# Kernel tuning notes

Measured on AMD Instinct MI355X. Metric: run time of the kernel, lower is better.

## Reference

```python
import jax, jax.numpy as jnp
import numpy as np

B, S, D = 32, 2048, 64
SQRT_DIM = float(np.sqrt(D))  # scale=True -> divide by sqrt(dim)


def setup_inputs() -> dict:
    key = jax.random.key(0)
    kq, kk, kv, km = jax.random.split(key, 4)
    query = jax.random.normal(kq, (B, S, D), dtype=jnp.float32)
    key_t = jax.random.normal(kk, (B, S, D), dtype=jnp.float32)
    value = jax.random.normal(kv, (B, S, D), dtype=jnp.float32)
    mask = jax.random.randint(km, (B, S, S), 0, 2).astype(jnp.bool_)
    return {"query": query, "key": key_t, "value": value, "mask": mask}


def reference(query, key, value, mask):
    # score = Q @ K^T / sqrt(dim)   -> [B, S, S]
    score = jnp.einsum('bqd,bkd->bqk', query, key) / SQRT_DIM
    score = jnp.where(mask, jnp.float32(-1e9), score)  # masked_fill_
    attn = jax.nn.softmax(score, axis=-1)
    # context = attn @ V   -> [B, S, D]  (block_mask is None -> no gamma)
    context = jnp.einsum('bqk,bkd->bqd', attn, value)
    return (context, attn)
```

## Files before the change

kernel.cpp:

```cpp
#include <hip/hip_runtime.h>
#include <hip/hip_bf16.h>

#define BB 32
#define SS 2048
#define DD 64
#define NTH 256
#define QT 16
#define KTL 128
#define SCALE 0.125f

typedef __attribute__((ext_vector_type(4))) float f32x4;
typedef __attribute__((ext_vector_type(8))) short bf16x8;

union B8 { bf16x8 v; unsigned int u[4]; };

__device__ __forceinline__ unsigned int pk2bf(float a, float b) {
    __hip_bfloat162 h = __float22bfloat162_rn(make_float2(a, b));
    unsigned int u;
    __builtin_memcpy(&u, &h, 4);
    return u;
}
__device__ __forceinline__ float bf_lo(unsigned int w) {
    return __builtin_bit_cast(float, w << 16);
}
__device__ __forceinline__ float bf_hi(unsigned int w) {
    return __builtin_bit_cast(float, w & 0xffff0000u);
}

__global__ __launch_bounds__(NTH, 3) void sdpa_mfma(
    const float* __restrict__ Q, const float* __restrict__ K,
    const float* __restrict__ V, const int* __restrict__ M,
    float* __restrict__ ctx, float* __restrict__ attn)
{
    __shared__ __align__(16) unsigned char smem[53248];
    unsigned short* k_lds = (unsigned short*)smem;
    unsigned int*   vt2   = (unsigned int*)(smem + 16384);
    unsigned short* bnc   = (unsigned short*)(smem + 49152);
    float*          scr   = (float*)smem;
    __shared__ float wsum[4][QT];
    __shared__ float inv_l[QT];

    const int t    = threadIdx.x;
    const int wave = t >> 6, l = t & 63, g = l >> 4, li = l & 15;
    const int b    = blockIdx.x >> 7;
    const int q0   = (blockIdx.x & 127) * QT;

    const float* Kb  = K + (size_t)b * SS * DD;
    const float* Vb  = V + (size_t)b * SS * DD;
    const int*   Mb  = M + ((size_t)b * SS + q0) * SS;
    float*      attb = attn + ((size_t)b * SS + q0) * SS;

    B8 qh[2], ql[2];
    {
        const float* qp = Q + ((size_t)(b * SS + q0 + li)) * DD + g * 8;
        #pragma unroll
        for (int h = 0; h < 2; ++h) {
            float f[8];
            *(float4*)&f[0] = *(const float4*)(qp + h * 32);
            *(float4*)&f[4] = *(const float4*)(qp + h * 32 + 4);
            #pragma unroll
            for (int i = 0; i < 4; ++i) {
                unsigned int hw = pk2bf(f[2*i], f[2*i+1]);
                qh[h].u[i] = hw;
                ql[h].u[i] = pk2bf(f[2*i] - bf_lo(hw), f[2*i+1] - bf_hi(hw));
            }
        }
    }

    auto stageK = [&](int tl) {
        const float4* Ks = (const float4*)(Kb + (size_t)tl * KTL * DD);
        #pragma unroll
        for (int i = 0; i < 8; ++i) {
            const int f4 = i * NTH + t;
            float4 kv = Ks[f4];
            const int kc = f4 >> 4, d4 = f4 & 15;
            const int by = (kc * 128 + d4 * 8) ^ ((kc & 7) << 4);
            uint2 wv;
            wv.x = pk2bf(kv.x, kv.y);
            wv.y = pk2bf(kv.z, kv.w);
            *(uint2*)((unsigned char*)k_lds + by) = wv;
        }
    };

    auto qk = [&](f32x4& s0, f32x4& s1) {
        const int kc0 = wave * 32 + li, kc1 = kc0 + 16;
        #pragma unroll
        for (int h = 0; h < 2; ++h) {
            const int off = h * 64 + g * 16;
            B8 kb0, kb1;
            kb0.v = *(const bf16x8*)((unsigned char*)k_lds + ((kc0 * 128 + off) ^ ((kc0 & 7) << 4)));
            kb1.v = *(const bf16x8*)((unsigned char*)k_lds + ((kc1 * 128 + off) ^ ((kc1 & 7) << 4)));
            s0 = __builtin_amdgcn_mfma_f32_16x16x32_bf16(qh[h].v, kb0.v, s0, 0, 0, 0);
            s0 = __builtin_amdgcn_mfma_f32_16x16x32_bf16(ql[h].v, kb0.v, s0, 0, 0, 0);
            s1 = __builtin_amdgcn_mfma_f32_16x16x32_bf16(qh[h].v, kb1.v, s1, 0, 0, 0);
            s1 = __builtin_amdgcn_mfma_f32_16x16x32_bf16(ql[h].v, kb1.v, s1, 0, 0, 0);
        }
    };

    float lsum[4] = {0.f, 0.f, 0.f, 0.f};
    unsigned int mb0 = 0, mb1 = 0, mb2 = 0, mb3 = 0;

    #pragma unroll 1
    for (int tl = 0; tl < 16; ++tl) {
        __syncthreads();
        stageK(tl);
        __syncthreads();
        const int kg0 = tl * KTL + wave * 32 + li;
        int m0a[4], m1a[4];
        #pragma unroll
        for (int r = 0; r < 4; ++r) {
            const size_t mo = (size_t)(g * 4 + r) * SS + kg0;
            m0a[r] = __builtin_nontemporal_load(&Mb[mo]);
            m1a[r] = __builtin_nontemporal_load(&Mb[mo + 16]);
        }
        f32x4 s0 = {0.f,0.f,0.f,0.f}, s1 = {0.f,0.f,0.f,0.f};
        qk(s0, s1);
        unsigned int fl = 0;
        #pragma unroll
        for (int r = 0; r < 4; ++r) {
            float e0 = __expf(s0[r] * SCALE);
            float e1 = __expf(s1[r] * SCALE);
            if (m0a[r]) { fl |= 1u << r;       e0 = 0.f; }
            if (m1a[r]) { fl |= 1u << (4 + r); e1 = 0.f; }
            lsum[r] += e0 + e1;
        }
        mb0 = (mb0 >> 8) | (mb1 << 24);
        mb1 = (mb1 >> 8) | (mb2 << 24);
        mb2 = (mb2 >> 8) | (mb3 << 24);
        mb3 = (mb3 >> 8) | (fl << 24);
    }

    #pragma unroll
    for (int off = 8; off >= 1; off >>= 1)
        #pragma unroll
        for (int r = 0; r < 4; ++r)
            lsum[r] += __shfl_xor(lsum[r], off, 64);
    if (li == 0) {
        #pragma unroll
        for (int r = 0; r < 4; ++r) wsum[wave][g * 4 + r] = lsum[r];
    }
    __syncthreads();
    if (t < QT) inv_l[t] = 1.0f / (wsum[0][t] + wsum[1][t] + wsum[2][t] + wsum[3][t]);
    __syncthreads();
    float invl[4];
    #pragma unroll
    for (int r = 0; r < 4; ++r) invl[r] = inv_l[g * 4 + r];

    f32x4 cacc[4] = {{0.f,0.f,0.f,0.f},{0.f,0.f,0.f,0.f},{0.f,0.f,0.f,0.f},{0.f,0.f,0.f,0.f}};
    unsigned short* bw = bnc + wave * 512;

    #pragma unroll 1
    for (int tl = 0; tl < 16; ++tl) {
        __syncthreads();
        stageK(tl);
        {
            const float4* Vs = (const float4*)(Vb + (size_t)tl * KTL * DD);
            #pragma unroll
            for (int i = 0; i < 4; ++i) {
                const int task = i * NTH + t;
                const int d4 = task & 15, k0 = (task >> 4) * 2;
                float4 va = Vs[k0 * 16 + d4];
                float4 vb = Vs[k0 * 16 + 16 + d4];
                const float* pa = (const float*)&va;
                const float* pb = (const float*)&vb;
                #pragma unroll
                for (int ww = 0; ww < 4; ++ww) {
                    const int d = d4 * 4 + ww;
                    unsigned int hp = pk2bf(pa[ww], pb[ww]);
                    unsigned int lp = pk2bf(pa[ww] - bf_lo(hp), pb[ww] - bf_hi(hp));
                    uint2 wv;
                    wv.x = (hp & 0xffffu) | (lp << 16);
                    wv.y = (hp >> 16) | (lp & 0xffff0000u);
                    const int widx = (d * 128 + k0) ^ (((d >> 2) & 7) << 2);
                    *(uint2*)&vt2[widx] = wv;
                }
            }
        }
        __syncthreads();
        f32x4 s0 = {0.f,0.f,0.f,0.f}, s1 = {0.f,0.f,0.f,0.f};
        qk(s0, s1);
        const unsigned int fl = mb0 & 0xffu;
        mb0 = (mb0 >> 8) | (mb1 << 24);
        mb1 = (mb1 >> 8) | (mb2 << 24);
        mb2 = (mb2 >> 8) | (mb3 << 24);
        mb3 >>= 8;
        const int kg0 = tl * KTL + wave * 32 + li;
        #pragma unroll
        for (int r = 0; r < 4; ++r) {
            float e0 = ((fl >> r)       & 1u) ? 0.f : __expf(s0[r] * SCALE);
            float e1 = ((fl >> (4 + r)) & 1u) ? 0.f : __expf(s1[r] * SCALE);
            const size_t ao = (size_t)(g * 4 + r) * SS + kg0;
            attb[ao]      = e0 * invl[r];
            attb[ao + 16] = e1 * invl[r];
            bw[((li >> 3) << 7)        + (g * 4 + r) * 8 + (li & 7)] = (unsigned short)pk2bf(e0, 0.f);
            bw[(((li + 16) >> 3) << 7) + (g * 4 + r) * 8 + (li & 7)] = (unsigned short)pk2bf(e1, 0.f);
        }
        B8 pf;
        pf.v = *(const bf16x8*)(bw + l * 8);
        #pragma unroll
        for (int c = 0; c < 4; ++c) {
            const int d    = c * 16 + li;
            const int base = d * 128 + wave * 32 + g * 8;
            const int sw   = ((d >> 2) & 7) << 2;
            uint4 wa = *(const uint4*)&vt2[(base) ^ sw];
            uint4 wb = *(const uint4*)&vt2[(base + 4) ^ sw];
            B8 vhf, vlf;
            vhf.u[0] = __builtin_amdgcn_perm(wa.y, wa.x, 0x05040100u);
            vlf.u[0] = __builtin_amdgcn_perm(wa.y, wa.x, 0x07060302u);
            vhf.u[1] = __builtin_amdgcn_perm(wa.w, wa.z, 0x05040100u);
            vlf.u[1] = __builtin_amdgcn_perm(wa.w, wa.z, 0x07060302u);
            vhf.u[2] = __builtin_amdgcn_perm(wb.y, wb.x, 0x05040100u);
            vlf.u[2] = __builtin_amdgcn_perm(wb.y, wb.x, 0x07060302u);
            vhf.u[3] = __builtin_amdgcn_perm(wb.w, wb.z, 0x05040100u);
            vlf.u[3] = __builtin_amdgcn_perm(wb.w, wb.z, 0x07060302u);
            cacc[c] = __builtin_amdgcn_mfma_f32_16x16x32_bf16(pf.v, vhf.v, cacc[c], 0, 0, 0);
            cacc[c] = __builtin_amdgcn_mfma_f32_16x16x32_bf16(pf.v, vlf.v, cacc[c], 0, 0, 0);
        }
    }

    __syncthreads();
    {
        const int row = wave * 64 + l;
        #pragma unroll
        for (int c = 0; c < 4; ++c)
            #pragma unroll
            for (int r = 0; r < 4; ++r)
                scr[row * 17 + c * 4 + r] = cacc[c][r];
    }
    __syncthreads();
    {
        const int q = t >> 4, d0 = (t & 15) * 4;
        float4 o;
        float* op = &o.x;
        #pragma unroll
        for (int dd = 0; dd < 4; ++dd) {
            const int d    = d0 + dd;
            const int lane = (q >> 2) * 16 + (d & 15);
            const int idx  = lane * 17 + (d >> 4) * 4 + (q & 3);
            float s = 0.f;
            #pragma unroll
            for (int w = 0; w < 4; ++w) s += scr[w * 64 * 17 + idx];
            op[dd] = s * inv_l[q];
        }
        *(float4*)(ctx + ((size_t)(b * SS + q0 + q)) * DD + d0) = o;
    }
}

extern "C" void kernel_launch(void* const* d_in, const int* in_sizes, int n_in,
                              void* d_out, int out_size, void* d_ws, size_t ws_size,
                              hipStream_t stream) {
    const float* Q = (const float*)d_in[0];
    const float* K = (const float*)d_in[1];
    const float* V = (const float*)d_in[2];
    const int*   M = (const int*)d_in[3];
    float* ctx  = (float*)d_out;
    float* attn = (float*)d_out + (size_t)BB * SS * DD;
    sdpa_mfma<<<dim3(BB * (SS / QT)), dim3(NTH), 0, stream>>>(Q, K, V, M, ctx, attn);
}
```

Baseline: 1.319 ms.

## Precompute bf16 K and split transposed V in prep kernels, read directly from global

Adds two prep kernels. One converts K to bf16 and the other transposes V into hi/lo bf16 planes, both written to workspace. The main kernel no longer stages K and V through LDS on every tile; it loads MFMA fragments straight from global/L2 and drops the per-tile barriers. LDS use shrinks enough to allow 4 blocks per CU, and the probability-bounce buffer gets an XOR swizzle. The cost is extra launches and workspace traffic, and K/V fragments are now reread from global memory by each of the 4096 blocks instead of being shared through LDS.

```diff
diff --git a/kernel.cpp b/kernel.cpp
--- a/kernel.cpp
+++ b/kernel.cpp
@@ -27,28 +27,77 @@
     return __builtin_bit_cast(float, w & 0xffff0000u);
 }
 
-__global__ __launch_bounds__(NTH, 3) void sdpa_mfma(
-    const float* __restrict__ Q, const float* __restrict__ K,
-    const float* __restrict__ V, const int* __restrict__ M,
+__global__ __launch_bounds__(NTH) void prepK(const float* __restrict__ K,
+                                             unsigned short* __restrict__ Kbf) {
+    const size_t i = (size_t)blockIdx.x * NTH + threadIdx.x;
+    const float4* s = (const float4*)K;
+    const float4 a = s[2 * i], c = s[2 * i + 1];
+    uint4 w;
+    w.x = pk2bf(a.x, a.y); w.y = pk2bf(a.z, a.w);
+    w.z = pk2bf(c.x, c.y); w.w = pk2bf(c.z, c.w);
+    ((uint4*)Kbf)[i] = w;
+}
+
+#define VPADF 68
+__global__ __launch_bounds__(NTH) void prepV(const float* __restrict__ V,
+                                             unsigned short* __restrict__ VTh,
+                                             unsigned short* __restrict__ VTl) {
+    __shared__ __align__(16) float lt[KTL * VPADF];
+    const int t  = threadIdx.x;
+    const int b  = blockIdx.x >> 4;
+    const int ck = blockIdx.x & 15;
+    const float4* Vs = (const float4*)(V + ((size_t)b * SS + ck * KTL) * DD);
+    #pragma unroll
+    for (int i = 0; i < 8; ++i) {
+        const int f4 = i * NTH + t;
+        float4 v = Vs[f4];
+        const int kc = f4 >> 4, d4 = f4 & 15;
+        *(float4*)&lt[kc * VPADF + d4 * 4] = v;
+    }
+    __syncthreads();
+    const int d = t >> 2, kseg = t & 3;
+    unsigned short* oh = VTh + ((size_t)b * DD + d) * SS + ck * KTL + kseg * 32;
+    unsigned short* ol = VTl + ((size_t)b * DD + d) * SS + ck * KTL + kseg * 32;
+    #pragma unroll
+    for (int cch = 0; cch < 4; ++cch) {
+        uint4 wh, wl;
+        unsigned int* ph = (unsigned int*)&wh;
+        unsigned int* pl = (unsigned int*)&wl;
+        #pragma unroll
+        for (int p = 0; p < 4; ++p) {
+            const int k0 = kseg * 32 + cch * 8 + p * 2;
+            const float a = lt[k0 * VPADF + d], c = lt[(k0 + 1) * VPADF + d];
+            const unsigned int hw = pk2bf(a, c);
+            ph[p] = hw;
+            pl[p] = pk2bf(a - bf_lo(hw), c - bf_hi(hw));
+        }
+        *(uint4*)(oh + cch * 8) = wh;
+        *(uint4*)(ol + cch * 8) = wl;
+    }
+}
+
+__global__ __launch_bounds__(NTH, 4) void sdpa_mfma2(
+    const float* __restrict__ Q, const int* __restrict__ M,
+    const unsigned short* __restrict__ Kbf,
+    const unsigned short* __restrict__ VTh, const unsigned short* __restrict__ VTl,
     float* __restrict__ ctx, float* __restrict__ attn)
 {
-    __shared__ __align__(16) unsigned char smem[53248];
-    unsigned short* k_lds = (unsigned short*)smem;
-    unsigned int*   vt2   = (unsigned int*)(smem + 16384);
-    unsigned short* bnc   = (unsigned short*)(smem + 49152);
-    float*          scr   = (float*)smem;
+    __shared__ __align__(16) unsigned char smem[17408];
     __shared__ float wsum[4][QT];
     __shared__ float inv_l[QT];
+    unsigned short* bnc = (unsigned short*)smem;
+    float*          scr = (float*)smem;
 
     const int t    = threadIdx.x;
     const int wave = t >> 6, l = t & 63, g = l >> 4, li = l & 15;
     const int b    = blockIdx.x >> 7;
     const int q0   = (blockIdx.x & 127) * QT;
 
-    const float* Kb  = K + (size_t)b * SS * DD;
-    const float* Vb  = V + (size_t)b * SS * DD;
-    const int*   Mb  = M + ((size_t)b * SS + q0) * SS;
-    float*      attb = attn + ((size_t)b * SS + q0) * SS;
+    const unsigned short* Kb  = Kbf + (size_t)b * SS * DD;
+    const unsigned short* Vhb = VTh + (size_t)b * DD * SS;
+    const unsigned short* Vlb = VTl + (size_t)b * DD * SS;
+    const int*   Mb   = M + ((size_t)b * SS + q0) * SS;
+    float*       attb = attn + ((size_t)b * SS + q0) * SS;
 
     B8 qh[2], ql[2];
     {
@@ -67,33 +116,19 @@
         }
     }
 
-    auto stageK = [&](int tl) {
-        const float4* Ks = (const float4*)(Kb + (size_t)tl * KTL * DD);
-        #pragma unroll
-        for (int i = 0; i < 8; ++i) {
-            const int f4 = i * NTH + t;
-            float4 kv = Ks[f4];
-            const int kc = f4 >> 4, d4 = f4 & 15;
-            const int by = (kc * 128 + d4 * 8) ^ ((kc & 7) << 4);
-            uint2 wv;
-            wv.x = pk2bf(kv.x, kv.y);
-            wv.y = pk2bf(kv.z, kv.w);
-            *(uint2*)((unsigned char*)k_lds + by) = wv;
-        }
-    };
-
-    auto qk = [&](f32x4& s0, f32x4& s1) {
-        const int kc0 = wave * 32 + li, kc1 = kc0 + 16;
+    const unsigned short* kf0 = Kb + (size_t)(wave * 32 + li) * DD + g * 8;
+
+    auto qk = [&](int tl, f32x4& s0, f32x4& s1) {
+        const unsigned short* p0 = kf0 + (size_t)tl * KTL * DD;
         #pragma unroll
         for (int h = 0; h < 2; ++h) {
-            const int off = h * 64 + g * 16;
-            B8 kb0, kb1;
-            kb0.v = *(const bf16x8*)((unsigned char*)k_lds + ((kc0 * 128 + off) ^ ((kc0 & 7) << 4)));
-            kb1.v = *(const bf16x8*)((unsigned char*)k_lds + ((kc1 * 128 + off) ^ ((kc1 & 7) << 4)));
-            s0 = __builtin_amdgcn_mfma_f32_16x16x32_bf16(qh[h].v, kb0.v, s0, 0, 0, 0);
-            s0 = __builtin_amdgcn_mfma_f32_16x16x32_bf16(ql[h].v, kb0.v, s0, 0, 0, 0);
-            s1 = __builtin_amdgcn_mfma_f32_16x16x32_bf16(qh[h].v, kb1.v, s1, 0, 0, 0);
-            s1 = __builtin_amdgcn_mfma_f32_16x16x32_bf16(ql[h].v, kb1.v, s1, 0, 0, 0);
+            B8 k0, k1;
+            k0.v = *(const bf16x8*)(p0 + 32 * h);
+            k1.v = *(const bf16x8*)(p0 + 16 * DD + 32 * h);
+            s0 = __builtin_amdgcn_mfma_f32_16x16x32_bf16(qh[h].v, k0.v, s0, 0, 0, 0);
+            s0 = __builtin_amdgcn_mfma_f32_16x16x32_bf16(ql[h].v, k0.v, s0, 0, 0, 0);
+            s1 = __builtin_amdgcn_mfma_f32_16x16x32_bf16(qh[h].v, k1.v, s1, 0, 0, 0);
+            s1 = __builtin_amdgcn_mfma_f32_16x16x32_bf16(ql[h].v, k1.v, s1, 0, 0, 0);
         }
     };
 
@@ -102,9 +137,6 @@
 
     #pragma unroll 1
     for (int tl = 0; tl < 16; ++tl) {
-        __syncthreads();
-        stageK(tl);
-        __syncthreads();
         const int kg0 = tl * KTL + wave * 32 + li;
         int m0a[4], m1a[4];
         #pragma unroll
@@ -114,7 +146,7 @@
             m1a[r] = __builtin_nontemporal_load(&Mb[mo + 16]);
         }
         f32x4 s0 = {0.f,0.f,0.f,0.f}, s1 = {0.f,0.f,0.f,0.f};
-        qk(s0, s1);
+        qk(tl, s0, s1);
         unsigned int fl = 0;
         #pragma unroll
         for (int r = 0; r < 4; ++r) {
@@ -151,34 +183,8 @@
 
     #pragma unroll 1
     for (int tl = 0; tl < 16; ++tl) {
-        __syncthreads();
-        stageK(tl);
-        {
-            const float4* Vs = (const float4*)(Vb + (size_t)tl * KTL * DD);
-            #pragma unroll
-            for (int i = 0; i < 4; ++i) {
-                const int task = i * NTH + t;
-                const int d4 = task & 15, k0 = (task >> 4) * 2;
-                float4 va = Vs[k0 * 16 + d4];
-                float4 vb = Vs[k0 * 16 + 16 + d4];
-                const float* pa = (const float*)&va;
-                const float* pb = (const float*)&vb;
-                #pragma unroll
-                for (int ww = 0; ww < 4; ++ww) {
-                    const int d = d4 * 4 + ww;
-                    unsigned int hp = pk2bf(pa[ww], pb[ww]);
-                    unsigned int lp = pk2bf(pa[ww] - bf_lo(hp), pb[ww] - bf_hi(hp));
-                    uint2 wv;
-                    wv.x = (hp & 0xffffu) | (lp << 16);
-                    wv.y = (hp >> 16) | (lp & 0xffff0000u);
-                    const int widx = (d * 128 + k0) ^ (((d >> 2) & 7) << 2);
-                    *(uint2*)&vt2[widx] = wv;
-                }
-            }
-        }
-        __syncthreads();
         f32x4 s0 = {0.f,0.f,0.f,0.f}, s1 = {0.f,0.f,0.f,0.f};
-        qk(s0, s1);
+        qk(tl, s0, s1);
         const unsigned int fl = mb0 & 0xffu;
         mb0 = (mb0 >> 8) | (mb1 << 24);
         mb1 = (mb1 >> 8) | (mb2 << 24);
@@ -192,29 +198,22 @@
             const size_t ao = (size_t)(g * 4 + r) * SS + kg0;
             attb[ao]      = e0 * invl[r];
             attb[ao + 16] = e1 * invl[r];
-            bw[((li >> 3) << 7)        + (g * 4 + r) * 8 + (li & 7)] = (unsigned short)pk2bf(e0, 0.f);
-            bw[(((li + 16) >> 3) << 7) + (g * 4 + r) * 8 + (li & 7)] = (unsigned short)pk2bf(e1, 0.f);
+            const int q = g * 4 + r;
+            const int b0 = li >> 3, b1 = (li + 16) >> 3;
+            bw[((b0 * 16 + (q ^ b0)) << 3) + (li & 7)] = (unsigned short)pk2bf(e0, 0.f);
+            bw[((b1 * 16 + (q ^ b1)) << 3) + (li & 7)] = (unsigned short)pk2bf(e1, 0.f);
         }
         B8 pf;
-        pf.v = *(const bf16x8*)(bw + l * 8);
+        pf.v = *(const bf16x8*)(bw + ((g * 16 + (li ^ g)) << 3));
+        const size_t vcol = (size_t)tl * KTL + wave * 32 + g * 8;
         #pragma unroll
         for (int c = 0; c < 4; ++c) {
-            const int d    = c * 16 + li;
-            const int base = d * 128 + wave * 32 + g * 8;
-            const int sw   = ((d >> 2) & 7) << 2;
-            uint4 wa = *(const uint4*)&vt2[(base) ^ sw];
-            uint4 wb = *(const uint4*)&vt2[(base + 4) ^ sw];
-            B8 vhf, vlf;
-            vhf.u[0] = __builtin_amdgcn_perm(wa.y, wa.x, 0x05040100u);
-            vlf.u[0] = __builtin_amdgcn_perm(wa.y, wa.x, 0x07060302u);
-            vhf.u[1] = __builtin_amdgcn_perm(wa.w, wa.z, 0x05040100u);
-            vlf.u[1] = __builtin_amdgcn_perm(wa.w, wa.z, 0x07060302u);
-            vhf.u[2] = __builtin_amdgcn_perm(wb.y, wb.x, 0x05040100u);
-            vlf.u[2] = __builtin_amdgcn_perm(wb.y, wb.x, 0x07060302u);
-            vhf.u[3] = __builtin_amdgcn_perm(wb.w, wb.z, 0x05040100u);
-            vlf.u[3] = __builtin_amdgcn_perm(wb.w, wb.z, 0x07060302u);
-            cacc[c] = __builtin_amdgcn_mfma_f32_16x16x32_bf16(pf.v, vhf.v, cacc[c], 0, 0, 0);
-            cacc[c] = __builtin_amdgcn_mfma_f32_16x16x32_bf16(pf.v, vlf.v, cacc[c], 0, 0, 0);
+            const size_t voff = (size_t)(c * 16 + li) * SS + vcol;
+            B8 vh, vl;
+            vh.v = *(const bf16x8*)(Vhb + voff);
+            vl.v = *(const bf16x8*)(Vlb + voff);
+            cacc[c] = __builtin_amdgcn_mfma_f32_16x16x32_bf16(pf.v, vh.v, cacc[c], 0, 0, 0);
+            cacc[c] = __builtin_amdgcn_mfma_f32_16x16x32_bf16(pf.v, vl.v, cacc[c], 0, 0, 0);
         }
     }
 
@@ -255,5 +254,13 @@
     const int*   M = (const int*)d_in[3];
     float* ctx  = (float*)d_out;
     float* attn = (float*)d_out + (size_t)BB * SS * DD;
-    sdpa_mfma<<<dim3(BB * (SS / QT)), dim3(NTH), 0, stream>>>(Q, K, V, M, ctx, attn);
-}
+
+    const size_t NE = (size_t)BB * SS * DD;
+    unsigned short* Kbf = (unsigned short*)d_ws;
+    unsigned short* VTh = Kbf + NE;
+    unsigned short* VTl = VTh + NE;
+
+    prepK<<<dim3((unsigned)(NE / 8 / NTH)), dim3(NTH), 0, stream>>>(K, Kbf);
+    prepV<<<dim3(BB * (SS / KTL)), dim3(NTH), 0, stream>>>(V, VTh, VTl);
+    sdpa_mfma2<<<dim3(BB * (SS / QT)), dim3(NTH), 0, stream>>>(Q, M, Kbf, VTh, VTl, ctx, attn);
+}
```

After: 1.287 ms. 1.03x faster.
